# Performance work log

Measured on AMD Instinct MI355X. Metric: run time of the kernel, lower is better.

The kernel has to match this reference:

```python
import jax, jax.numpy as jnp
import numpy as np

D_MODEL = 1024
NUM_HEADS = 16
HEAD_DIM = D_MODEL // NUM_HEADS


def setup_inputs() -> dict:
    key = jax.random.key(0)
    ks = jax.random.split(key, 9)
    B, S, D = 4, 2048, D_MODEL
    scale = 1.0 / np.sqrt(D)
    x = jax.random.normal(ks[0], (B, S, D), dtype=jnp.float32)
    wq = jax.random.normal(ks[1], (D, D), dtype=jnp.float32) * scale
    wk = jax.random.normal(ks[2], (D, D), dtype=jnp.float32) * scale
    wv = jax.random.normal(ks[3], (D, D), dtype=jnp.float32) * scale
    wo = jax.random.normal(ks[4], (D, D), dtype=jnp.float32) * scale
    bq = jax.random.normal(ks[5], (D,), dtype=jnp.float32) * 0.02
    bk = jax.random.normal(ks[6], (D,), dtype=jnp.float32) * 0.02
    bv = jax.random.normal(ks[7], (D,), dtype=jnp.float32) * 0.02
    bo = jax.random.normal(ks[8], (D,), dtype=jnp.float32) * 0.02
    return {"x": x, "wq": wq, "bq": bq, "wk": wk, "bk": bk,
            "wv": wv, "bv": bv, "wo": wo, "bo": bo}


def _split_heads(t):  # [B,S,D] -> [B,H,S,Dh]
    B, S, _ = t.shape
    return t.reshape(B, S, NUM_HEADS, HEAD_DIM).transpose(0, 2, 1, 3)


def reference(x, wq, bq, wk, bk, wv, bv, wo, bo):
    B, S, D = x.shape
    q = _split_heads(x @ wq + bq)  # [B,H,S,Dh]
    k = _split_heads(x @ wk + bk)
    v = _split_heads(x @ wv + bv)
    scores = jnp.einsum("bhqd,bhkd->bhqk", q, k) / jnp.sqrt(
        jnp.asarray(HEAD_DIM, dtype=x.dtype))
    causal = jnp.tril(jnp.ones((S, S), dtype=bool))  # [S,S]
    scores = jnp.where(causal, scores, jnp.finfo(scores.dtype).min)
    attn = jax.nn.softmax(scores, axis=-1)
    ctx = jnp.einsum("bhqk,bhkd->bhqd", attn, v)  # [B,H,S,Dh]
    ctx = ctx.transpose(0, 2, 1, 3).reshape(B, S, D)
    return ctx @ wo + bo
```

## Files before the change

kernel.cpp:

```cpp
#include <hip/hip_runtime.h>
#include <hip/hip_bf16.h>
#include <stdint.h>

#define DMODEL 1024
#define NH 16
#define DH 64
#define BATCH 4
#define SEQ 2048

#if __has_builtin(__builtin_amdgcn_exp2f)
#define EXP2F(x) __builtin_amdgcn_exp2f(x)
#else
#define EXP2F(x) exp2f(x)
#endif

typedef __attribute__((ext_vector_type(8))) short short8;
typedef __attribute__((ext_vector_type(4))) float f32x4;
typedef __attribute__((ext_vector_type(4))) ushort ushort4v;

__device__ __forceinline__ ushort f2bf(float f) {
    union { float f; unsigned u; } v; v.f = f;
    unsigned r = v.u + 0x7fffu + ((v.u >> 16) & 1u);
    return (ushort)(r >> 16);
}

__global__ __launch_bounds__(256) void convert_bf16(const float* __restrict__ src,
                                                    ushort* __restrict__ dst) {
    const size_t i = ((size_t)blockIdx.x * 256 + threadIdx.x) * 8;
    float4 a = *(const float4*)(src + i);
    float4 b = *(const float4*)(src + i + 4);
    short8 r;
    r[0] = (short)f2bf(a.x); r[1] = (short)f2bf(a.y);
    r[2] = (short)f2bf(a.z); r[3] = (short)f2bf(a.w);
    r[4] = (short)f2bf(b.x); r[5] = (short)f2bf(b.y);
    r[6] = (short)f2bf(b.z); r[7] = (short)f2bf(b.w);
    *(short8*)(dst + i) = r;
}

__global__ __launch_bounds__(256) void transpose_cvt_w4(
    const float* __restrict__ s0, const float* __restrict__ s1,
    const float* __restrict__ s2, const float* __restrict__ s3,
    ushort* __restrict__ d0, ushort* __restrict__ d1,
    ushort* __restrict__ d2, ushort* __restrict__ d3) {
    __shared__ ushort tile[64][65];
    const int z = blockIdx.z;
    const float* src = (z == 0) ? s0 : (z == 1) ? s1 : (z == 2) ? s2 : s3;
    ushort* dst = (z == 0) ? d0 : (z == 1) ? d1 : (z == 2) ? d2 : d3;
    const int bx = blockIdx.x * 64;
    const int by = blockIdx.y * 64;
    const int tx = threadIdx.x & 63, ty = threadIdx.x >> 6;
    #pragma unroll
    for (int i = 0; i < 64; i += 4)
        tile[ty + i][tx] = f2bf(src[(size_t)(by + ty + i) * DMODEL + bx + tx]);
    __syncthreads();
    #pragma unroll
    for (int i = 0; i < 64; i += 4)
        dst[(size_t)(bx + ty + i) * DMODEL + by + tx] = tile[tx][ty + i];
}

template <int MODE>
__global__ __launch_bounds__(256) void gemm_bt(
    const ushort* __restrict__ A, const ushort* __restrict__ Bt,
    const float* __restrict__ b0, const float* __restrict__ b1,
    const float* __restrict__ b2,
    void* __restrict__ o0v, void* __restrict__ o1v, void* __restrict__ o2v) {
    __shared__ __align__(16) ushort smem[8192];
    const int lane = threadIdx.x & 63;
    const int wv   = threadIdx.x >> 6;
    const int mBase = blockIdx.y * 128;
    const int nBase = blockIdx.x * 128;
    const int wm = (wv >> 1) * 64;
    const int wn = (wv & 1) * 64;

    f32x4 acc[4][4];
    #pragma unroll
    for (int i = 0; i < 4; ++i)
        #pragma unroll
        for (int j = 0; j < 4; ++j) acc[i][j] = (f32x4){0.f, 0.f, 0.f, 0.f};

    const int lrow = lane >> 2;
    const int lcol = (lane & 3) * 8;
    const int frow = lane & 15;
    const int fcol = (lane >> 4) * 8;

    for (int k0 = 0; k0 < DMODEL; k0 += 32) {
        #pragma unroll
        for (int i = 0; i < 2; ++i) {
            const int c = wv * 2 + i;
            const ushort* ga = A + (size_t)(mBase + c * 16 + lrow) * DMODEL + k0 + lcol;
            __builtin_amdgcn_global_load_lds(
                (const __attribute__((address_space(1))) void*)ga,
                (__attribute__((address_space(3))) void*)&smem[c * 512], 16, 0, 0);
            const ushort* gb = Bt + (size_t)(nBase + c * 16 + lrow) * DMODEL + k0 + lcol;
            __builtin_amdgcn_global_load_lds(
                (const __attribute__((address_space(1))) void*)gb,
                (__attribute__((address_space(3))) void*)&smem[4096 + c * 512], 16, 0, 0);
        }
        __syncthreads();
        short8 af[4], bfr[4];
        #pragma unroll
        for (int t = 0; t < 4; ++t)
            af[t] = *(const short8*)&smem[(wm + t * 16 + frow) * 32 + fcol];
        #pragma unroll
        for (int t = 0; t < 4; ++t)
            bfr[t] = *(const short8*)&smem[4096 + (wn + t * 16 + frow) * 32 + fcol];
        #pragma unroll
        for (int i = 0; i < 4; ++i)
            #pragma unroll
            for (int j = 0; j < 4; ++j)
                acc[i][j] = __builtin_amdgcn_mfma_f32_16x16x32_bf16(af[i], bfr[j],
                                                                   acc[i][j], 0, 0, 0);
        __syncthreads();
    }

    const int orow = (lane >> 4) * 4;
    const int ocol = lane & 15;

    if (MODE == 1) {
        #pragma unroll
        for (int i = 0; i < 4; ++i)
            #pragma unroll
            for (int j = 0; j < 4; ++j)
                #pragma unroll
                for (int r = 0; r < 4; ++r) {
                    const int m = mBase + wm + i * 16 + orow + r;
                    const int n = nBase + wn + j * 16 + ocol;
                    ((float*)o0v)[(size_t)m * DMODEL + n] = acc[i][j][r] + b0[n];
                }
        return;
    }

    ushort* sw = &smem[wv * 2048];
    const int mat = nBase >> 10;
    const int nb0 = (nBase & 1023) + wn;
    const int hb  = nb0 >> 6;
    const float* bp = (mat == 0) ? b0 : ((mat == 1) ? b1 : b2);
    float bj[4];
    #pragma unroll
    for (int j = 0; j < 4; ++j) bj[j] = bp[nb0 + j * 16 + ocol];
    const int bbq = (mBase + wm) >> 11;
    const int s0w = (mBase + wm) & 2047;
    const float qscale = (mat == 0) ? 0.1803368801f : 1.0f;

    if (mat < 2) {
        ushort* obase = (ushort*)((mat == 0) ? o0v : o1v) +
                        ((size_t)(bbq * NH + hb) * SEQ + s0w) * DH;
        const int row = lane >> 2, cc = lane & 3;
        #pragma unroll
        for (int i = 0; i < 4; ++i) {
            #pragma unroll
            for (int j = 0; j < 4; ++j)
                #pragma unroll
                for (int r = 0; r < 4; ++r)
                    sw[(orow + r) * 72 + j * 16 + ocol] =
                        f2bf((acc[i][j][r] + bj[j]) * qscale);
            asm volatile("s_waitcnt lgkmcnt(0)" ::: "memory");
            #pragma unroll
            for (int p = 0; p < 2; ++p) {
                short8 v8 = *(const short8*)&sw[row * 72 + cc * 8 + p * 32];
                *(short8*)&obase[(size_t)(i * 16 + row) * DH + cc * 8 + p * 32] = v8;
            }
            asm volatile("s_waitcnt lgkmcnt(0)" ::: "memory");
        }
    } else {
        ushort* op = (ushort*)o2v;
        const int rowd = lane >> 2, sc = lane & 3;
        #pragma unroll
        for (int j = 0; j < 4; ++j) {
            #pragma unroll
            for (int i = 0; i < 4; ++i)
                #pragma unroll
                for (int r = 0; r < 4; ++r)
                    sw[ocol * 72 + i * 16 + orow + r] = f2bf(acc[i][j][r] + bj[j]);
            asm volatile("s_waitcnt lgkmcnt(0)" ::: "memory");
            ushort* vbase = op + ((size_t)(bbq * NH + hb) * DH + j * 16 + rowd) * SEQ + s0w;
            #pragma unroll
            for (int p = 0; p < 2; ++p) {
                short8 v8 = *(const short8*)&sw[rowd * 72 + sc * 8 + p * 32];
                *(short8*)&vbase[sc * 8 + p * 32] = v8;
            }
            asm volatile("s_waitcnt lgkmcnt(0)" ::: "memory");
        }
    }
}

#define PSTR 72
__global__ __launch_bounds__(256, 4) void flash_attn(
    const ushort* __restrict__ Q, const ushort* __restrict__ K,
    const ushort* __restrict__ Vt, ushort* __restrict__ ctx) {
    __shared__ __align__(16) ushort Ks[4096];
    __shared__ __align__(16) ushort Vs[4096];
    __shared__ __align__(16) ushort plds[4][16 * PSTR];
    const int lane = threadIdx.x & 63;
    const int wv   = threadIdx.x >> 6;
    const int bh   = blockIdx.x & 63;
    const int Jp   = blockIdx.x >> 6;
    const int bb = bh >> 4, h = bh & 15;

    const ushort* Qb = Q + (size_t)bh * SEQ * DH;
    const ushort* Kb = K + (size_t)bh * SEQ * DH;
    const ushort* Vb = Vt + (size_t)bh * DH * SEQ;

    const int frow = lane & 15;
    const int fq   = lane >> 4;
    const int r7s  = lane >> 3;
    const int csw  = (lane & 7) ^ r7s;

    short8 ones;
    #pragma unroll
    for (int i = 0; i < 8; ++i) ones[i] = (short)0x3F80;

    #pragma unroll 1
    for (int half = 0; half < 2; ++half) {
        const int Je = half ? (31 - Jp) : Jp;
        const int q0 = Je * 64 + wv * 16;
        const int qmax = q0 + 15;

        short8 qf[2];
        #pragma unroll
        for (int ks = 0; ks < 2; ++ks)
            qf[ks] = *(const short8*)&Qb[(size_t)(q0 + frow) * DH + ks * 32 + fq * 8];

        f32x4 o[4], lacc;
        #pragma unroll
        for (int t = 0; t < 4; ++t) o[t] = (f32x4){0.f, 0.f, 0.f, 0.f};
        lacc = (f32x4){0.f, 0.f, 0.f, 0.f};

        #pragma unroll 1
        for (int it = 0; it <= Je; ++it) {
            const int k0 = it * 64;
            __syncthreads();
            #pragma unroll
            for (int i = 0; i < 2; ++i) {
                const int c = wv * 2 + i;
                const ushort* gk = Kb + (size_t)(k0 + c * 8 + r7s) * DH + csw * 8;
                __builtin_amdgcn_global_load_lds(
                    (const __attribute__((address_space(1))) void*)gk,
                    (__attribute__((address_space(3))) void*)&Ks[c * 512], 16, 0, 0);
                const ushort* gv = Vb + (size_t)(c * 8 + r7s) * SEQ + k0 + csw * 8;
                __builtin_amdgcn_global_load_lds(
                    (const __attribute__((address_space(1))) void*)gv,
                    (__attribute__((address_space(3))) void*)&Vs[c * 512], 16, 0, 0);
            }
            __syncthreads();

            if (it < Je) {
                f32x4 sacc[4];
                #pragma unroll
                for (int nt = 0; nt < 4; ++nt) sacc[nt] = (f32x4){0.f, 0.f, 0.f, 0.f};
                #pragma unroll
                for (int nt = 0; nt < 4; ++nt) {
                    const int row = nt * 16 + frow, r7 = row & 7;
                    #pragma unroll
                    for (int ks = 0; ks < 2; ++ks) {
                        short8 kf = *(const short8*)
                            &Ks[(row >> 3) * 512 + r7 * 64 + (((ks * 4 + fq) ^ r7) * 8)];
                        sacc[nt] = __builtin_amdgcn_mfma_f32_16x16x32_bf16(kf, qf[ks],
                                                                          sacc[nt], 0, 0, 0);
                    }
                }
                #pragma unroll
                for (int nt = 0; nt < 4; ++nt) {
                    float p0 = EXP2F(sacc[nt][0]);
                    float p1 = EXP2F(sacc[nt][1]);
                    float p2 = EXP2F(sacc[nt][2]);
                    float p3 = EXP2F(sacc[nt][3]);
                    uint2 dw;
                    dw.x = __builtin_amdgcn_perm(__float_as_uint(p1), __float_as_uint(p0),
                                                 0x07060302u);
                    dw.y = __builtin_amdgcn_perm(__float_as_uint(p3), __float_as_uint(p2),
                                                 0x07060302u);
                    *(uint2*)&plds[wv][frow * PSTR + nt * 16 + fq * 4] = dw;
                }
                asm volatile("s_waitcnt lgkmcnt(0)" ::: "memory");
                #pragma unroll
                for (int kc = 0; kc < 2; ++kc) {
                    short8 pf = *(const short8*)&plds[wv][frow * PSTR + kc * 32 + fq * 8];
                    lacc = __builtin_amdgcn_mfma_f32_16x16x32_bf16(ones, pf, lacc, 0, 0, 0);
                    #pragma unroll
                    for (int t = 0; t < 4; ++t) {
                        const int row = t * 16 + frow, r7 = row & 7;
                        short8 vf = *(const short8*)
                            &Vs[(row >> 3) * 512 + r7 * 64 + (((kc * 4 + fq) ^ r7) * 8)];
                        o[t] = __builtin_amdgcn_mfma_f32_16x16x32_bf16(vf, pf, o[t], 0, 0, 0);
                    }
                }
            } else {
                const int qrow = q0 + frow;
                f32x4 sacc[4];
                #pragma unroll
                for (int nt = 0; nt < 4; ++nt) sacc[nt] = (f32x4){0.f, 0.f, 0.f, 0.f};
                #pragma unroll
                for (int nt = 0; nt < 4; ++nt)
                    if (k0 + nt * 16 <= qmax) {
                        const int row = nt * 16 + frow, r7 = row & 7;
                        #pragma unroll
                        for (int ks = 0; ks < 2; ++ks) {
                            short8 kf = *(const short8*)
                                &Ks[(row >> 3) * 512 + r7 * 64 + (((ks * 4 + fq) ^ r7) * 8)];
                            sacc[nt] = __builtin_amdgcn_mfma_f32_16x16x32_bf16(kf, qf[ks],
                                                                              sacc[nt], 0, 0, 0);
                        }
                    }
                #pragma unroll
                for (int nt = 0; nt < 4; ++nt) {
                    uint2 dw; dw.x = 0u; dw.y = 0u;
                    if (k0 + nt * 16 <= qmax) {
                        float pp[4];
                        #pragma unroll
                        for (int r = 0; r < 4; ++r) {
                            const float e = EXP2F(sacc[nt][r]);
                            pp[r] = (k0 + nt * 16 + fq * 4 + r <= qrow) ? e : 0.f;
                        }
                        dw.x = __builtin_amdgcn_perm(__float_as_uint(pp[1]),
                                                     __float_as_uint(pp[0]), 0x07060302u);
                        dw.y = __builtin_amdgcn_perm(__float_as_uint(pp[3]),
                                                     __float_as_uint(pp[2]), 0x07060302u);
                    }
                    *(uint2*)&plds[wv][frow * PSTR + nt * 16 + fq * 4] = dw;
                }
                asm volatile("s_waitcnt lgkmcnt(0)" ::: "memory");
                #pragma unroll
                for (int kc = 0; kc < 2; ++kc) {
                    if (k0 + kc * 32 <= qmax) {
                        short8 pf = *(const short8*)&plds[wv][frow * PSTR + kc * 32 + fq * 8];
                        lacc = __builtin_amdgcn_mfma_f32_16x16x32_bf16(ones, pf, lacc, 0, 0, 0);
                        #pragma unroll
                        for (int t = 0; t < 4; ++t) {
                            const int row = t * 16 + frow, r7 = row & 7;
                            short8 vf = *(const short8*)
                                &Vs[(row >> 3) * 512 + r7 * 64 + (((kc * 4 + fq) ^ r7) * 8)];
                            o[t] = __builtin_amdgcn_mfma_f32_16x16x32_bf16(vf, pf, o[t], 0, 0, 0);
                        }
                    }
                }
            }
        }
        const float inv = 1.0f / lacc[0];
        const int qrow = q0 + frow;
        ushort* cp = ctx + (size_t)(bb * SEQ + qrow) * DMODEL + h * DH;
        #pragma unroll
        for (int t = 0; t < 4; ++t) {
            ushort4v ov;
            #pragma unroll
            for (int r = 0; r < 4; ++r) ov[r] = f2bf(o[t][r] * inv);
            *(ushort4v*)&cp[t * 16 + fq * 4] = ov;
        }
    }
}

extern "C" void kernel_launch(void* const* d_in, const int* in_sizes, int n_in,
                              void* d_out, int out_size, void* d_ws, size_t ws_size,
                              hipStream_t stream) {
    const float* x  = (const float*)d_in[0];
    const float* wq = (const float*)d_in[1];
    const float* bq = (const float*)d_in[2];
    const float* wk = (const float*)d_in[3];
    const float* bk = (const float*)d_in[4];
    const float* wvp = (const float*)d_in[5];
    const float* bv = (const float*)d_in[6];
    const float* wo = (const float*)d_in[7];
    const float* bo = (const float*)d_in[8];
    float* out = (float*)d_out;
    ushort* ws = (ushort*)d_ws;

    const size_t QSZ = (size_t)BATCH * NH * SEQ * DH;
    ushort* xbf   = ws;
    ushort* qws   = ws + QSZ;
    ushort* kws   = ws + 2 * QSZ;
    ushort* vtws  = ws + 3 * QSZ;
    ushort* ctxws = ws + 4 * QSZ;
    ushort* wtqkv = ws + 5 * QSZ;
    ushort* wto   = wtqkv + 3 * (size_t)DMODEL * DMODEL;

    dim3 tb(256);
    convert_bf16<<<dim3(4096), tb, 0, stream>>>(x, xbf);
    transpose_cvt_w4<<<dim3(16, 16, 4), tb, 0, stream>>>(
        wq, wk, wvp, wo,
        wtqkv, wtqkv + (size_t)DMODEL * DMODEL, wtqkv + 2 * (size_t)DMODEL * DMODEL, wto);

    gemm_bt<0><<<dim3(24, 64), tb, 0, stream>>>(xbf, wtqkv, bq, bk, bv,
                                                qws, kws, vtws);
    flash_attn<<<dim3(1024), tb, 0, stream>>>(qws, kws, vtws, ctxws);
    gemm_bt<1><<<dim3(8, 64), tb, 0, stream>>>(ctxws, wto, bo, nullptr, nullptr,
                                               out, nullptr, nullptr);
}
```

Baseline: 257.1 us.

## Replace QKV projection GEMM with 256x256 tiled, double-buffered direct-to-LDS kernel

Adds a dedicated QKV projection kernel with 256x256 output tiles, 512 threads, and BK=64. It stages A and B with global_load_lds into XOR-swizzled, double-buffered LDS and interleaves loads with MFMA quarters under s_setprio and barriers. It also remaps block IDs for L2 locality. The larger tiles raise arithmetic intensity and are meant to hide global latency, at the cost of 128KB of LDS, heavy register use and only 384 blocks.

```diff
diff --git a/kernel.cpp b/kernel.cpp
--- a/kernel.cpp
+++ b/kernel.cpp
@@ -58,6 +58,223 @@
         dst[(size_t)(bx + ty + i) * DMODEL + by + tx] = tile[tx][ty + i];
 }
 
+#define BK 64
+#define NT 16
+
+__global__ __launch_bounds__(512, 2) void gemm_qkv(
+    const ushort* __restrict__ A, const ushort* __restrict__ Bt,
+    const float* __restrict__ b0, const float* __restrict__ b1,
+    const float* __restrict__ b2,
+    ushort* __restrict__ o0, ushort* __restrict__ o1, ushort* __restrict__ o2) {
+    __shared__ __align__(16) ushort lds[65536];
+    const int tid  = threadIdx.x;
+    const int lane = tid & 63;
+    const int wv   = tid >> 6;
+
+    const int bid = blockIdx.x;
+    const int w   = (bid & 7) * 48 + (bid >> 3);
+    const int by  = w / 12, bx = w - by * 12;
+    const int mBase = by * 256, nBase = bx * 256;
+
+    const int wmh = wv >> 2;
+    const int wn4 = wv & 3;
+    const int wbh = wn4 >> 1;
+    const int nbh = (wn4 & 1) * 64;
+
+    const int frow = lane & 15;
+    const int fq   = lane >> 4;
+
+    const int trow = tid >> 3;
+    const int tcho = ((tid & 7) ^ (trow & 7)) * 8;
+    const ushort* gA = A  + (size_t)(mBase + trow) * DMODEL + tcho;
+    const ushort* gB = Bt + (size_t)(nBase + trow) * DMODEL + tcho;
+    const int ldsw = wv * 512;
+
+    f32x4 acc[8][4];
+    #pragma unroll
+    for (int i = 0; i < 8; ++i)
+        #pragma unroll
+        for (int j = 0; j < 4; ++j) acc[i][j] = (f32x4){0.f, 0.f, 0.f, 0.f};
+
+#define STG(gp, off) __builtin_amdgcn_global_load_lds( \
+    (const __attribute__((address_space(1))) void*)(gp), \
+    (__attribute__((address_space(3))) void*)&lds[(off) + ldsw], 16, 0, 0)
+#define STAGE_A(u, h) { const ushort* g_ = gA + (size_t)((h) * 128) * DMODEL + (u) * BK; \
+    STG(g_, ((u) & 1) * 32768 + (h) * 8192); \
+    STG(g_ + (size_t)64 * DMODEL, ((u) & 1) * 32768 + (h) * 8192 + 4096); }
+#define STAGE_B(u, h) { const ushort* g_ = gB + (size_t)((h) * 128) * DMODEL + (u) * BK; \
+    STG(g_, ((u) & 1) * 32768 + 16384 + (h) * 8192); \
+    STG(g_ + (size_t)64 * DMODEL, ((u) & 1) * 32768 + 16384 + (h) * 8192 + 4096); }
+
+    STAGE_B(0, 0); STAGE_B(0, 1);
+    STAGE_A(0, 0); STAGE_A(0, 1);
+    STAGE_B(1, 0); STAGE_B(1, 1);
+    asm volatile("s_waitcnt vmcnt(4)" ::: "memory");
+    __builtin_amdgcn_s_barrier();
+
+    short8 af[4][2], bf0[2][2], bf1[2][2];
+
+    #pragma unroll 1
+    for (int u = 0; u < NT; ++u) {
+        const int b = u & 1;
+        const ushort* bufA = &lds[b * 32768 + wmh * 8192];
+        const ushort* bufB = &lds[b * 32768 + 16384 + wbh * 8192];
+
+        #pragma unroll
+        for (int f = 0; f < 4; ++f) {
+            const int ra = f * 16 + frow;
+            #pragma unroll
+            for (int ks = 0; ks < 2; ++ks)
+                af[f][ks] = *(const short8*)&bufA[ra * 64 + (((ks * 4 + fq) ^ (ra & 7)) << 3)];
+        }
+        #pragma unroll
+        for (int f2 = 0; f2 < 2; ++f2) {
+            const int rb = nbh + f2 * 16 + frow;
+            #pragma unroll
+            for (int ks = 0; ks < 2; ++ks)
+                bf0[f2][ks] = *(const short8*)&bufB[rb * 64 + (((ks * 4 + fq) ^ (rb & 7)) << 3)];
+        }
+        if (u + 1 < NT) STAGE_A(u + 1, 0);
+        __builtin_amdgcn_s_barrier();
+        asm volatile("s_waitcnt lgkmcnt(0)" ::: "memory");
+        __builtin_amdgcn_s_setprio(1);
+        #pragma unroll
+        for (int f = 0; f < 4; ++f)
+            #pragma unroll
+            for (int f2 = 0; f2 < 2; ++f2)
+                #pragma unroll
+                for (int ks = 0; ks < 2; ++ks)
+                    acc[f][f2] = __builtin_amdgcn_mfma_f32_16x16x32_bf16(
+                        af[f][ks], bf0[f2][ks], acc[f][f2], 0, 0, 0);
+        __builtin_amdgcn_s_setprio(0);
+        __builtin_amdgcn_s_barrier();
+
+        #pragma unroll
+        for (int f2 = 0; f2 < 2; ++f2) {
+            const int rb = nbh + 32 + f2 * 16 + frow;
+            #pragma unroll
+            for (int ks = 0; ks < 2; ++ks)
+                bf1[f2][ks] = *(const short8*)&bufB[rb * 64 + (((ks * 4 + fq) ^ (rb & 7)) << 3)];
+        }
+        if (u + 1 < NT) STAGE_A(u + 1, 1);
+        __builtin_amdgcn_s_barrier();
+        asm volatile("s_waitcnt lgkmcnt(0)" ::: "memory");
+        __builtin_amdgcn_s_setprio(1);
+        #pragma unroll
+        for (int f = 0; f < 4; ++f)
+            #pragma unroll
+            for (int f2 = 0; f2 < 2; ++f2)
+                #pragma unroll
+                for (int ks = 0; ks < 2; ++ks)
+                    acc[f][2 + f2] = __builtin_amdgcn_mfma_f32_16x16x32_bf16(
+                        af[f][ks], bf1[f2][ks], acc[f][2 + f2], 0, 0, 0);
+        __builtin_amdgcn_s_setprio(0);
+        __builtin_amdgcn_s_barrier();
+
+        #pragma unroll
+        for (int f = 0; f < 4; ++f) {
+            const int ra = 64 + f * 16 + frow;
+            #pragma unroll
+            for (int ks = 0; ks < 2; ++ks)
+                af[f][ks] = *(const short8*)&bufA[ra * 64 + (((ks * 4 + fq) ^ (ra & 7)) << 3)];
+        }
+        if (u + 2 < NT) STAGE_B(u + 2, 0);
+        __builtin_amdgcn_s_barrier();
+        asm volatile("s_waitcnt lgkmcnt(0)" ::: "memory");
+        __builtin_amdgcn_s_setprio(1);
+        #pragma unroll
+        for (int f = 0; f < 4; ++f)
+            #pragma unroll
+            for (int f2 = 0; f2 < 2; ++f2)
+                #pragma unroll
+                for (int ks = 0; ks < 2; ++ks)
+                    acc[4 + f][2 + f2] = __builtin_amdgcn_mfma_f32_16x16x32_bf16(
+                        af[f][ks], bf1[f2][ks], acc[4 + f][2 + f2], 0, 0, 0);
+        __builtin_amdgcn_s_setprio(0);
+        __builtin_amdgcn_s_barrier();
+
+        if (u + 2 < NT) STAGE_B(u + 2, 1);
+        __builtin_amdgcn_s_barrier();
+        __builtin_amdgcn_s_setprio(1);
+        #pragma unroll
+        for (int f = 0; f < 4; ++f)
+            #pragma unroll
+            for (int f2 = 0; f2 < 2; ++f2)
+                #pragma unroll
+                for (int ks = 0; ks < 2; ++ks)
+                    acc[4 + f][f2] = __builtin_amdgcn_mfma_f32_16x16x32_bf16(
+                        af[f][ks], bf0[f2][ks], acc[4 + f][f2], 0, 0, 0);
+        __builtin_amdgcn_s_setprio(0);
+        if (u + 2 < NT) { asm volatile("s_waitcnt vmcnt(4)" ::: "memory"); }
+        else            { asm volatile("s_waitcnt vmcnt(0)" ::: "memory"); }
+        __builtin_amdgcn_s_barrier();
+    }
+#undef STG
+#undef STAGE_A
+#undef STAGE_B
+
+    __syncthreads();
+    const int orow = fq * 4;
+    const int ocol = frow;
+    ushort* sw = &lds[wv * 1152];
+    const int mat = nBase >> 10;
+    const int nb0 = (nBase & 1023) + wn4 * 64;
+    const int hb  = nb0 >> 6;
+    const float* bp = (mat == 0) ? b0 : ((mat == 1) ? b1 : b2);
+    float bj[4];
+    #pragma unroll
+    for (int j = 0; j < 4; ++j) bj[j] = bp[nb0 + j * 16 + ocol];
+    const int mrow = mBase + wmh * 128;
+    const int bbq = mrow >> 11;
+    const int s0w = mrow & 2047;
+    const float qscale = (mat == 0) ? 0.1803368801f : 1.0f;
+
+    if (mat < 2) {
+        ushort* obase = ((mat == 0) ? o0 : o1) +
+                        ((size_t)(bbq * NH + hb) * SEQ + s0w) * DH;
+        const int row = lane >> 2, cc = lane & 3;
+        #pragma unroll
+        for (int i = 0; i < 8; ++i) {
+            #pragma unroll
+            for (int j = 0; j < 4; ++j)
+                #pragma unroll
+                for (int r = 0; r < 4; ++r)
+                    sw[(orow + r) * 72 + j * 16 + ocol] =
+                        f2bf((acc[i][j][r] + bj[j]) * qscale);
+            asm volatile("s_waitcnt lgkmcnt(0)" ::: "memory");
+            #pragma unroll
+            for (int p = 0; p < 2; ++p) {
+                short8 v8 = *(const short8*)&sw[row * 72 + cc * 8 + p * 32];
+                *(short8*)&obase[(size_t)(i * 16 + row) * DH + cc * 8 + p * 32] = v8;
+            }
+            asm volatile("s_waitcnt lgkmcnt(0)" ::: "memory");
+        }
+    } else {
+        const int rowd = lane >> 2, sc = lane & 3;
+        #pragma unroll
+        for (int j = 0; j < 4; ++j) {
+            #pragma unroll
+            for (int ih = 0; ih < 2; ++ih) {
+                #pragma unroll
+                for (int ii = 0; ii < 4; ++ii)
+                    #pragma unroll
+                    for (int r = 0; r < 4; ++r)
+                        sw[ocol * 72 + ii * 16 + orow + r] =
+                            f2bf(acc[ih * 4 + ii][j][r] + bj[j]);
+                asm volatile("s_waitcnt lgkmcnt(0)" ::: "memory");
+                ushort* vbase = o2 + ((size_t)(bbq * NH + hb) * DH + j * 16 + rowd) * SEQ +
+                                s0w + ih * 64;
+                #pragma unroll
+                for (int p = 0; p < 2; ++p) {
+                    short8 v8 = *(const short8*)&sw[rowd * 72 + sc * 8 + p * 32];
+                    *(short8*)&vbase[sc * 8 + p * 32] = v8;
+                }
+                asm volatile("s_waitcnt lgkmcnt(0)" ::: "memory");
+            }
+        }
+    }
+}
+
 template <int MODE>
 __global__ __launch_bounds__(256) void gemm_bt(
     const ushort* __restrict__ A, const ushort* __restrict__ Bt,
@@ -128,59 +345,6 @@
                     ((float*)o0v)[(size_t)m * DMODEL + n] = acc[i][j][r] + b0[n];
                 }
         return;
-    }
-
-    ushort* sw = &smem[wv * 2048];
-    const int mat = nBase >> 10;
-    const int nb0 = (nBase & 1023) + wn;
-    const int hb  = nb0 >> 6;
-    const float* bp = (mat == 0) ? b0 : ((mat == 1) ? b1 : b2);
-    float bj[4];
-    #pragma unroll
-    for (int j = 0; j < 4; ++j) bj[j] = bp[nb0 + j * 16 + ocol];
-    const int bbq = (mBase + wm) >> 11;
-    const int s0w = (mBase + wm) & 2047;
-    const float qscale = (mat == 0) ? 0.1803368801f : 1.0f;
-
-    if (mat < 2) {
-        ushort* obase = (ushort*)((mat == 0) ? o0v : o1v) +
-                        ((size_t)(bbq * NH + hb) * SEQ + s0w) * DH;
-        const int row = lane >> 2, cc = lane & 3;
-        #pragma unroll
-        for (int i = 0; i < 4; ++i) {
-            #pragma unroll
-            for (int j = 0; j < 4; ++j)
-                #pragma unroll
-                for (int r = 0; r < 4; ++r)
-                    sw[(orow + r) * 72 + j * 16 + ocol] =
-                        f2bf((acc[i][j][r] + bj[j]) * qscale);
-            asm volatile("s_waitcnt lgkmcnt(0)" ::: "memory");
-            #pragma unroll
-            for (int p = 0; p < 2; ++p) {
-                short8 v8 = *(const short8*)&sw[row * 72 + cc * 8 + p * 32];
-                *(short8*)&obase[(size_t)(i * 16 + row) * DH + cc * 8 + p * 32] = v8;
-            }
-            asm volatile("s_waitcnt lgkmcnt(0)" ::: "memory");
-        }
-    } else {
-        ushort* op = (ushort*)o2v;
-        const int rowd = lane >> 2, sc = lane & 3;
-        #pragma unroll
-        for (int j = 0; j < 4; ++j) {
-            #pragma unroll
-            for (int i = 0; i < 4; ++i)
-                #pragma unroll
-                for (int r = 0; r < 4; ++r)
-                    sw[ocol * 72 + i * 16 + orow + r] = f2bf(acc[i][j][r] + bj[j]);
-            asm volatile("s_waitcnt lgkmcnt(0)" ::: "memory");
-            ushort* vbase = op + ((size_t)(bbq * NH + hb) * DH + j * 16 + rowd) * SEQ + s0w;
-            #pragma unroll
-            for (int p = 0; p < 2; ++p) {
-                short8 v8 = *(const short8*)&sw[rowd * 72 + sc * 8 + p * 32];
-                *(short8*)&vbase[sc * 8 + p * 32] = v8;
-            }
-            asm volatile("s_waitcnt lgkmcnt(0)" ::: "memory");
-        }
     }
 }
 
@@ -379,8 +543,8 @@
         wq, wk, wvp, wo,
         wtqkv, wtqkv + (size_t)DMODEL * DMODEL, wtqkv + 2 * (size_t)DMODEL * DMODEL, wto);
 
-    gemm_bt<0><<<dim3(24, 64), tb, 0, stream>>>(xbf, wtqkv, bq, bk, bv,
-                                                qws, kws, vtws);
+    gemm_qkv<<<dim3(384), dim3(512), 0, stream>>>(xbf, wtqkv, bq, bk, bv,
+                                                  qws, kws, vtws);
     flash_attn<<<dim3(1024), tb, 0, stream>>>(qws, kws, vtws, ctxws);
     gemm_bt<1><<<dim3(8, 64), tb, 0, stream>>>(ctxws, wto, bo, nullptr, nullptr,
                                                out, nullptr, nullptr);
```

After: 250.0 us. -2.8%, faster.

## Rewrite GEMMs with 256x128 tiles, triple-buffered LDS, swizzle and block remap

Applied to the files above, without the earlier changes.

Replaces the single-buffered 128x128 bf16 GEMM with a 512-thread, 256x128-tile kernel. It uses BK=64, a three-stage LDS ring filled by global_load_lds two iterations ahead, an XOR-swizzled LDS layout to avoid bank conflicts, split MFMA phases under s_setprio, and a block-index remap for L2 locality. The goal is to hide global-load latency and raise MFMA utilisation in the QKV and output projections. In exchange it uses 144KB of LDS per block, which limits occupancy, and relies on hand-tuned vmcnt waits that must exactly match the number of loads in flight.

```diff
diff --git a/kernel.cpp b/kernel.cpp
--- a/kernel.cpp
+++ b/kernel.cpp
@@ -58,19 +58,38 @@
         dst[(size_t)(bx + ty + i) * DMODEL + by + tx] = tile[tx][ty + i];
 }
 
+#define BK 64
+#define NT 16
+
 template <int MODE>
-__global__ __launch_bounds__(256) void gemm_bt(
+__global__ __launch_bounds__(512, 2) void gemm_tile(
     const ushort* __restrict__ A, const ushort* __restrict__ Bt,
     const float* __restrict__ b0, const float* __restrict__ b1,
     const float* __restrict__ b2,
     void* __restrict__ o0v, void* __restrict__ o1v, void* __restrict__ o2v) {
-    __shared__ __align__(16) ushort smem[8192];
-    const int lane = threadIdx.x & 63;
-    const int wv   = threadIdx.x >> 6;
-    const int mBase = blockIdx.y * 128;
-    const int nBase = blockIdx.x * 128;
+    __shared__ __align__(16) ushort lds[73728];
+    const int tid  = threadIdx.x;
+    const int lane = tid & 63;
+    const int wv   = tid >> 6;
+
+    const int bid = blockIdx.x;
+    const int by  = 4 * (bid & 7) + ((bid >> 3) & 3);
+    const int bx  = bid >> 5;
+    const int mBase = by * 256, nBase = bx * 128;
+
     const int wm = (wv >> 1) * 64;
     const int wn = (wv & 1) * 64;
+    const int frow = lane & 15;
+    const int fq   = lane >> 4;
+    const int r7   = frow & 7;
+    const int sw0  = (fq ^ r7) << 3;
+    const int sw1  = ((4 + fq) ^ r7) << 3;
+
+    const int trow = tid >> 3;
+    const int tcho = ((tid & 7) ^ (trow & 7)) * 8;
+    const ushort* gA = A  + (size_t)(mBase + trow) * DMODEL + tcho;
+    const ushort* gB = Bt + (size_t)(nBase + trow) * DMODEL + tcho;
+    const int ldsw = wv * 512;
 
     f32x4 acc[4][4];
     #pragma unroll
@@ -78,43 +97,93 @@
         #pragma unroll
         for (int j = 0; j < 4; ++j) acc[i][j] = (f32x4){0.f, 0.f, 0.f, 0.f};
 
-    const int lrow = lane >> 2;
-    const int lcol = (lane & 3) * 8;
-    const int frow = lane & 15;
-    const int fcol = (lane >> 4) * 8;
-
-    for (int k0 = 0; k0 < DMODEL; k0 += 32) {
-        #pragma unroll
-        for (int i = 0; i < 2; ++i) {
-            const int c = wv * 2 + i;
-            const ushort* ga = A + (size_t)(mBase + c * 16 + lrow) * DMODEL + k0 + lcol;
-            __builtin_amdgcn_global_load_lds(
-                (const __attribute__((address_space(1))) void*)ga,
-                (__attribute__((address_space(3))) void*)&smem[c * 512], 16, 0, 0);
-            const ushort* gb = Bt + (size_t)(nBase + c * 16 + lrow) * DMODEL + k0 + lcol;
-            __builtin_amdgcn_global_load_lds(
-                (const __attribute__((address_space(1))) void*)gb,
-                (__attribute__((address_space(3))) void*)&smem[4096 + c * 512], 16, 0, 0);
-        }
-        __syncthreads();
-        short8 af[4], bfr[4];
-        #pragma unroll
-        for (int t = 0; t < 4; ++t)
-            af[t] = *(const short8*)&smem[(wm + t * 16 + frow) * 32 + fcol];
-        #pragma unroll
-        for (int t = 0; t < 4; ++t)
-            bfr[t] = *(const short8*)&smem[4096 + (wn + t * 16 + frow) * 32 + fcol];
-        #pragma unroll
-        for (int i = 0; i < 4; ++i)
-            #pragma unroll
-            for (int j = 0; j < 4; ++j)
-                acc[i][j] = __builtin_amdgcn_mfma_f32_16x16x32_bf16(af[i], bfr[j],
-                                                                   acc[i][j], 0, 0, 0);
-        __syncthreads();
+#define STG(gp, off) __builtin_amdgcn_global_load_lds( \
+    (const __attribute__((address_space(1))) void*)(gp), \
+    (__attribute__((address_space(3))) void*)&lds[(off) + ldsw], 16, 0, 0)
+#define STAGE_A(sb, u, h) STG(gA + (size_t)(h) * 64 * DMODEL + (u) * BK, \
+                              (sb) + (h) * 4096)
+#define STAGE_B(sb, u, h) STG(gB + (size_t)(h) * 64 * DMODEL + (u) * BK, \
+                              (sb) + 16384 + (h) * 4096)
+
+    STAGE_A(0, 0, 0); STAGE_A(0, 0, 1); STAGE_A(0, 0, 2); STAGE_A(0, 0, 3);
+    STAGE_B(0, 0, 0); STAGE_B(0, 0, 1);
+    STAGE_A(24576, 1, 0); STAGE_A(24576, 1, 1); STAGE_A(24576, 1, 2);
+    STAGE_A(24576, 1, 3); STAGE_B(24576, 1, 0); STAGE_B(24576, 1, 1);
+    asm volatile("s_waitcnt vmcnt(6)" ::: "memory");
+    __builtin_amdgcn_s_barrier();
+
+    int sc = 0;
+    #pragma unroll 1
+    for (int u = 0; u < NT; ++u) {
+        const int scB = sc * 24576;
+        const int sp  = (sc == 0) ? 2 : sc - 1;
+        const int spB = sp * 24576;
+        const ushort* bufA = &lds[scB + wm * 64];
+        const ushort* bufB = &lds[scB + 16384 + wn * 64];
+
+        short8 af[4][2], bf[2][2];
+
+        #pragma unroll
+        for (int f = 0; f < 4; ++f) {
+            const int ro = (f * 16 + frow) * 64;
+            af[f][0] = *(const short8*)&bufA[ro + sw0];
+            af[f][1] = *(const short8*)&bufA[ro + sw1];
+        }
+        #pragma unroll
+        for (int f2 = 0; f2 < 2; ++f2) {
+            const int ro = (f2 * 16 + frow) * 64;
+            bf[f2][0] = *(const short8*)&bufB[ro + sw0];
+            bf[f2][1] = *(const short8*)&bufB[ro + sw1];
+        }
+        if (u + 2 < NT) {
+            STAGE_A(spB, u + 2, 0); STAGE_A(spB, u + 2, 1); STAGE_A(spB, u + 2, 2);
+        }
+        __builtin_amdgcn_s_barrier();
+        asm volatile("s_waitcnt lgkmcnt(0)" ::: "memory");
+        __builtin_amdgcn_s_setprio(1);
+        #pragma unroll
+        for (int f = 0; f < 4; ++f)
+            #pragma unroll
+            for (int f2 = 0; f2 < 2; ++f2)
+                #pragma unroll
+                for (int ks = 0; ks < 2; ++ks)
+                    acc[f][f2] = __builtin_amdgcn_mfma_f32_16x16x32_bf16(
+                        af[f][ks], bf[f2][ks], acc[f][f2], 0, 0, 0);
+        __builtin_amdgcn_s_setprio(0);
+        __builtin_amdgcn_s_barrier();
+
+        #pragma unroll
+        for (int f2 = 0; f2 < 2; ++f2) {
+            const int ro = (32 + f2 * 16 + frow) * 64;
+            bf[f2][0] = *(const short8*)&bufB[ro + sw0];
+            bf[f2][1] = *(const short8*)&bufB[ro + sw1];
+        }
+        if (u + 2 < NT) {
+            STAGE_A(spB, u + 2, 3); STAGE_B(spB, u + 2, 0); STAGE_B(spB, u + 2, 1);
+        }
+        __builtin_amdgcn_s_barrier();
+        asm volatile("s_waitcnt lgkmcnt(0)" ::: "memory");
+        __builtin_amdgcn_s_setprio(1);
+        #pragma unroll
+        for (int f = 0; f < 4; ++f)
+            #pragma unroll
+            for (int f2 = 0; f2 < 2; ++f2)
+                #pragma unroll
+                for (int ks = 0; ks < 2; ++ks)
+                    acc[f][2 + f2] = __builtin_amdgcn_mfma_f32_16x16x32_bf16(
+                        af[f][ks], bf[f2][ks], acc[f][2 + f2], 0, 0, 0);
+        __builtin_amdgcn_s_setprio(0);
+        if (u + 2 < NT)       { asm volatile("s_waitcnt vmcnt(6)" ::: "memory"); }
+        else if (u + 2 == NT) { asm volatile("s_waitcnt vmcnt(0)" ::: "memory"); }
+        __builtin_amdgcn_s_barrier();
+        sc = (sc == 2) ? 0 : sc + 1;
     }
-
-    const int orow = (lane >> 4) * 4;
-    const int ocol = lane & 15;
+#undef STG
+#undef STAGE_A
+#undef STAGE_B
+
+    const int orow = fq * 4;
+    const int ocol = frow;
 
     if (MODE == 1) {
         #pragma unroll
@@ -130,7 +199,9 @@
         return;
     }
 
-    ushort* sw = &smem[wv * 2048];
+    __syncthreads();
+    ushort* o0 = (ushort*)o0v; ushort* o1 = (ushort*)o1v; ushort* o2 = (ushort*)o2v;
+    ushort* sw = &lds[wv * 1152];
     const int mat = nBase >> 10;
     const int nb0 = (nBase & 1023) + wn;
     const int hb  = nb0 >> 6;
@@ -138,12 +209,13 @@
     float bj[4];
     #pragma unroll
     for (int j = 0; j < 4; ++j) bj[j] = bp[nb0 + j * 16 + ocol];
-    const int bbq = (mBase + wm) >> 11;
-    const int s0w = (mBase + wm) & 2047;
+    const int mrow = mBase + wm;
+    const int bbq = mrow >> 11;
+    const int s0w = mrow & 2047;
     const float qscale = (mat == 0) ? 0.1803368801f : 1.0f;
 
     if (mat < 2) {
-        ushort* obase = (ushort*)((mat == 0) ? o0v : o1v) +
+        ushort* obase = ((mat == 0) ? o0 : o1) +
                         ((size_t)(bbq * NH + hb) * SEQ + s0w) * DH;
         const int row = lane >> 2, cc = lane & 3;
         #pragma unroll
@@ -163,21 +235,20 @@
             asm volatile("s_waitcnt lgkmcnt(0)" ::: "memory");
         }
     } else {
-        ushort* op = (ushort*)o2v;
-        const int rowd = lane >> 2, sc = lane & 3;
+        const int rowd = lane >> 2, scl = lane & 3;
         #pragma unroll
         for (int j = 0; j < 4; ++j) {
             #pragma unroll
-            for (int i = 0; i < 4; ++i)
+            for (int ii = 0; ii < 4; ++ii)
                 #pragma unroll
                 for (int r = 0; r < 4; ++r)
-                    sw[ocol * 72 + i * 16 + orow + r] = f2bf(acc[i][j][r] + bj[j]);
+                    sw[ocol * 72 + ii * 16 + orow + r] = f2bf(acc[ii][j][r] + bj[j]);
             asm volatile("s_waitcnt lgkmcnt(0)" ::: "memory");
-            ushort* vbase = op + ((size_t)(bbq * NH + hb) * DH + j * 16 + rowd) * SEQ + s0w;
+            ushort* vbase = o2 + ((size_t)(bbq * NH + hb) * DH + j * 16 + rowd) * SEQ + s0w;
             #pragma unroll
             for (int p = 0; p < 2; ++p) {
-                short8 v8 = *(const short8*)&sw[rowd * 72 + sc * 8 + p * 32];
-                *(short8*)&vbase[sc * 8 + p * 32] = v8;
+                short8 v8 = *(const short8*)&sw[rowd * 72 + scl * 8 + p * 32];
+                *(short8*)&vbase[scl * 8 + p * 32] = v8;
             }
             asm volatile("s_waitcnt lgkmcnt(0)" ::: "memory");
         }
@@ -379,9 +450,9 @@
         wq, wk, wvp, wo,
         wtqkv, wtqkv + (size_t)DMODEL * DMODEL, wtqkv + 2 * (size_t)DMODEL * DMODEL, wto);
 
-    gemm_bt<0><<<dim3(24, 64), tb, 0, stream>>>(xbf, wtqkv, bq, bk, bv,
-                                                qws, kws, vtws);
+    gemm_tile<0><<<dim3(768), dim3(512), 0, stream>>>(xbf, wtqkv, bq, bk, bv,
+                                                      qws, kws, vtws);
     flash_attn<<<dim3(1024), tb, 0, stream>>>(qws, kws, vtws, ctxws);
-    gemm_bt<1><<<dim3(8, 64), tb, 0, stream>>>(ctxws, wto, bo, nullptr, nullptr,
-                                               out, nullptr, nullptr);
-}
+    gemm_tile<1><<<dim3(256), dim3(512), 0, stream>>>(ctxws, wto, bo, nullptr, nullptr,
+                                                      out, nullptr, nullptr);
+}
```

New measurement: 242.5 us. 5.7% less time.
